# Kernel tuning notes

Hardware: AMD Instinct MI355X
Metric: run time of the kernel (lower is better)

## Reference

```python
import jax, jax.numpy as jnp
import numpy as np

FEATURE_DIM = 128  # user_aae.feature_dim == item_aae.feature_dim


def _encode(row, W1, b1, W2, b2):
    # row = [feature | x_rest]; original concatenates x and feature before the encoder MLP
    feat = row[:, :FEATURE_DIM]
    xr = row[:, FEATURE_DIM:]
    h = jax.nn.relu(jnp.concatenate([xr, feat], axis=-1) @ W1 + b1)
    return h @ W2 + b2  # [B, latent]


def setup_inputs() -> dict:
    key = jax.random.key(0)
    ks = jax.random.split(key, 12)
    B, NU, NI = 8192, 50000, 50000
    ROW, H, L = 2128, 512, 256  # feature_dim(128) + x_dim(2000)
    x = jnp.stack([
        jax.random.randint(ks[0], (B,), 0, NU),
        jax.random.randint(ks[1], (B,), 0, NI),
    ], axis=1).astype(jnp.int64)
    s1 = 1.0 / np.sqrt(ROW)
    s2 = 1.0 / np.sqrt(H)
    return {
        "x": x,
        "user_lookup": jax.random.normal(ks[2], (NU, ROW), jnp.float32),
        "item_lookup": jax.random.normal(ks[3], (NI, ROW), jnp.float32),
        "uW1": jax.random.normal(ks[4], (ROW, H), jnp.float32) * s1,
        "ub1": jnp.zeros((H,), jnp.float32),
        "uW2": jax.random.normal(ks[5], (H, L), jnp.float32) * s2,
        "ub2": jnp.zeros((L,), jnp.float32),
        "iW1": jax.random.normal(ks[6], (ROW, H), jnp.float32) * s1,
        "ib1": jnp.zeros((H,), jnp.float32),
        "iW2": jax.random.normal(ks[7], (H, L), jnp.float32) * s2,
        "ib2": jnp.zeros((L,), jnp.float32),
    }


def reference(x, user_lookup, item_lookup, uW1, ub1, uW2, ub2, iW1, ib1, iW2, ib2):
    user_row = user_lookup[x[:, 0]]  # [B, ROW]
    item_row = item_lookup[x[:, 1]]  # [B, ROW]
    u = _encode(user_row, uW1, ub1, uW2, ub2)  # [B, L]
    v = _encode(item_row, iW1, ib1, iW2, ib2)  # [B, L]
    # diag(u @ v.T) == rowwise dot product (identical math, no B x B matrix)
    diag = jnp.sum(u * v, axis=-1)
    return diag[:, None]  # [B, 1]
```

## Files before the change

kernel.cpp:

```cpp
#include <hip/hip_runtime.h>
#include <stdint.h>

typedef __attribute__((ext_vector_type(8))) short bf16x8;
typedef __attribute__((ext_vector_type(4))) float f32x4;

#define MFMA16(a, b, c) __builtin_amdgcn_mfma_f32_16x16x32_bf16((a), (b), (c), 0, 0, 0)

static __device__ __forceinline__ unsigned short f2bf(float f) {
  union { float f; unsigned int u; } cv;
  cv.f = f;
  return (unsigned short)((cv.u + 0x7fffu + ((cv.u >> 16) & 1u)) >> 16);
}

#define BATCH 8192
#define ROWD  2128
#define HID   512
#define LATD  256
#define KC1   272
#define NT1   68
#define HSL_TW (BATCH * HID)

__global__ __launch_bounds__(256) void ASAECF_tcast(
    const float* __restrict__ in0, const float* __restrict__ in1,
    unsigned short* __restrict__ out, int N, int lgN, int Kin, int KC, int perm)
{
  const float* __restrict__ in = blockIdx.z ? in1 : in0;
  unsigned short* __restrict__ o = out + (size_t)blockIdx.z * KC * N * 8;
  const int s = blockIdx.x * 256 + threadIdx.x;
  const int kc = s >> lgN, n = s & (N - 1);
  unsigned short v[8];
#pragma unroll
  for (int e = 0; e < 8; ++e) {
    const int k = kc * 8 + e;
    float f = 0.0f;
    if (k < Kin) {
      const int src = perm ? (k < 128 ? k + 2000 : k - 128) : k;
      f = in[(size_t)src * N + n];
    }
    v[e] = f2bf(f);
  }
  *(uint4*)(o + (size_t)s * 8) = *(const uint4*)v;
}

__global__ __launch_bounds__(512) void ASAECF_gemm1(
    const int* __restrict__ x,
    const float* __restrict__ ulook, const float* __restrict__ ilook,
    const unsigned short* __restrict__ w1s,
    const float* __restrict__ ub1, const float* __restrict__ ib1,
    unsigned short* __restrict__ hsl)
{
  const int bid   = blockIdx.x;
  const int xcd   = bid & 7;
  const int tower = xcd >> 2;
  const int rb    = (bid >> 3) * 4 + (xcd & 3);

  const float* __restrict__ look = tower ? ilook : ulook;
  const unsigned short* __restrict__ w1 = w1s + (size_t)tower * KC1 * HID * 8;
  const float* __restrict__ b1 = tower ? ib1 : ub1;
  unsigned short* __restrict__ hout = hsl + (size_t)tower * HSL_TW;

  __shared__ unsigned short Ab[2][64 * 40];

  const int tid  = threadIdx.x;
  const int lane = tid & 63, wid = tid >> 6;
  const int fr   = lane & 15, fq = lane >> 4;
  const int row0 = rb * 64;

  const int ar = tid >> 3, ak = (tid & 7) * 4;
  const long long arow = (long long)x[(row0 + ar) * 2 + tower] * ROWD + ak;

  int boff[4];
#pragma unroll
  for (int n = 0; n < 4; ++n)
    boff[n] = (fq * 512 + wid * 64 + n * 16 + fr) * 8;

  auto loadA = [&](int tt) -> f32x4 {
    f32x4 v = {0.0f, 0.0f, 0.0f, 0.0f};
    if (tt * 32 + ak <= ROWD - 4)
      v = __builtin_nontemporal_load((const f32x4*)(look + arow + tt * 32));
    return v;
  };
  auto writeA = [&](int buf, f32x4 v) {
    uint2 p;
    p.x = (unsigned)f2bf(v[0]) | ((unsigned)f2bf(v[1]) << 16);
    p.y = (unsigned)f2bf(v[2]) | ((unsigned)f2bf(v[3]) << 16);
    *(uint2*)&Ab[buf][ar * 40 + ak] = p;
  };

  f32x4 acc[4][4] = {};
  bf16x8 bgc[4], bgn[4];
  f32x4 rA0, rA1;

  writeA(0, loadA(0));
  rA0 = loadA(1);
  rA1 = loadA(2);
#pragma unroll
  for (int n = 0; n < 4; ++n) bgc[n] = *(const bf16x8*)(w1 + boff[n]);

#pragma unroll 2
  for (int t = 0; t < NT1; ++t) {
    __syncthreads();
    const int cu = t & 1;

    const unsigned short* bpn = w1 + (size_t)(t + 1) * (4 * 512 * 8);
#pragma unroll
    for (int n = 0; n < 4; ++n) bgn[n] = *(const bf16x8*)(bpn + boff[n]);

    bf16x8 af[4];
#pragma unroll
    for (int m = 0; m < 4; ++m)
      af[m] = *(const bf16x8*)&Ab[cu][(m * 16 + fr) * 40 + fq * 8];
#pragma unroll
    for (int n = 0; n < 4; ++n)
#pragma unroll
      for (int m = 0; m < 4; ++m)
        acc[m][n] = MFMA16(af[m], bgc[n], acc[m][n]);

    if (cu == 0) { writeA(1, rA0); rA0 = loadA(t + 3); }
    else         { writeA(0, rA1); rA1 = loadA(t + 3); }

#pragma unroll
    for (int n = 0; n < 4; ++n) bgc[n] = bgn[n];
  }

#pragma unroll
  for (int n = 0; n < 4; ++n) {
    const int col = wid * 64 + n * 16 + fr;
    const int kc = col >> 3, e = col & 7;
    const float bb = b1[col];
    unsigned short* hb = hout + (((size_t)rb * 64 + kc) * 64) * 8 + e;
#pragma unroll
    for (int m = 0; m < 4; ++m)
#pragma unroll
      for (int i = 0; i < 4; ++i) {
        const int row = m * 16 + fq * 4 + i;
        const float v = fmaxf(acc[m][n][i] + bb, 0.0f);
        hb[row * 8] = f2bf(v);
      }
  }
}

__global__ __launch_bounds__(512, 2) void ASAECF_gemm2dot(
    const unsigned short* __restrict__ hsl,
    const unsigned short* __restrict__ w2s,
    const float* __restrict__ ub2, const float* __restrict__ ib2,
    float* __restrict__ out)
{
  const int tid  = threadIdx.x;
  const int lane = tid & 63, wid = tid >> 6;
  const int fr   = lane & 15, fq = lane >> 4;
  const int rb   = blockIdx.x;
  const int row0 = rb * 32;

  const unsigned short* __restrict__ hu = hsl;
  const unsigned short* __restrict__ hv = hsl + (size_t)HSL_TW;
  const size_t abase = ((size_t)(rb >> 1) * 64) * 64 * 8;
  const int lrow0 = (rb & 1) * 32;

  f32x4 au[2][2] = {}, av[2][2] = {};

#pragma unroll
  for (int t = 0; t < 8; ++t) {
#pragma unroll
    for (int s = 0; s < 2; ++s) {
      const int kc = t * 8 + s * 4 + fq;
      bf16x8 a_u[2], a_v[2], b_u[2], b_v[2];
#pragma unroll
      for (int m = 0; m < 2; ++m) {
        const size_t off = abase + ((size_t)kc * 64 + lrow0 + m * 16 + fr) * 8;
        a_u[m] = *(const bf16x8*)(hu + off);
        a_v[m] = *(const bf16x8*)(hv + off);
      }
#pragma unroll
      for (int n = 0; n < 2; ++n) {
        const int col = wid * 32 + n * 16 + fr;
        const size_t offb = ((size_t)kc * 256 + col) * 8;
        b_u[n] = *(const bf16x8*)(w2s + offb);
        b_v[n] = *(const bf16x8*)(w2s + (size_t)64 * 256 * 8 + offb);
      }
#pragma unroll
      for (int m = 0; m < 2; ++m)
#pragma unroll
        for (int n = 0; n < 2; ++n) {
          au[m][n] = MFMA16(a_u[m], b_u[n], au[m][n]);
          av[m][n] = MFMA16(a_v[m], b_v[n], av[m][n]);
        }
    }
  }

  __shared__ float red[8][32];
  float bu[2], bv[2];
#pragma unroll
  for (int n = 0; n < 2; ++n) {
    const int col = wid * 32 + n * 16 + fr;
    bu[n] = ub2[col];
    bv[n] = ib2[col];
  }
#pragma unroll
  for (int m = 0; m < 2; ++m)
#pragma unroll
    for (int i = 0; i < 4; ++i) {
      float p = 0.0f;
#pragma unroll
      for (int n = 0; n < 2; ++n)
        p += (au[m][n][i] + bu[n]) * (av[m][n][i] + bv[n]);
      p += __shfl_xor(p, 1, 64);
      p += __shfl_xor(p, 2, 64);
      p += __shfl_xor(p, 4, 64);
      p += __shfl_xor(p, 8, 64);
      if (fr == 0) red[wid][m * 16 + fq * 4 + i] = p;
    }
  __syncthreads();
  if (tid < 32) {
    float s = 0.0f;
#pragma unroll
    for (int w = 0; w < 8; ++w) s += red[w][tid];
    out[row0 + tid] = s;
  }
}

extern "C" void kernel_launch(void* const* d_in, const int* in_sizes, int n_in,
                              void* d_out, int out_size, void* d_ws, size_t ws_size,
                              hipStream_t stream) {
  (void)in_sizes; (void)n_in; (void)out_size; (void)ws_size;
  const int*   x     = (const int*)d_in[0];
  const float* ulook = (const float*)d_in[1];
  const float* ilook = (const float*)d_in[2];
  const float* uW1   = (const float*)d_in[3];
  const float* ub1   = (const float*)d_in[4];
  const float* uW2   = (const float*)d_in[5];
  const float* ub2   = (const float*)d_in[6];
  const float* iW1   = (const float*)d_in[7];
  const float* ib1   = (const float*)d_in[8];
  const float* iW2   = (const float*)d_in[9];
  const float* ib2   = (const float*)d_in[10];
  float* out = (float*)d_out;

  char* ws = (char*)d_ws;
  unsigned short* w1s = (unsigned short*)(ws);
  unsigned short* w2s = (unsigned short*)(ws + 4456448);
  unsigned short* hsl = (unsigned short*)(ws + 4980736);

  ASAECF_tcast<<<dim3(544, 1, 2), 256, 0, stream>>>(uW1, iW1, w1s, 512, 9, ROWD, KC1, 1);
  ASAECF_tcast<<<dim3(64, 1, 2),  256, 0, stream>>>(uW2, iW2, w2s, 256, 8, HID, 64, 0);
  ASAECF_gemm1<<<dim3(256), 512, 0, stream>>>(x, ulook, ilook, w1s, ub1, ib1, hsl);
  ASAECF_gemm2dot<<<dim3(256), 512, 0, stream>>>(hsl, w2s, ub2, ib2, out);
}
```

Measured before the change: 89.37 us.

## Stage half-K gathered activation rows in large swizzled LDS before MFMA loop

The first GEMM now gathers all 64 rows of each block for half of the K range at once. It converts them to bf16 and stores them in about 136 KB of dynamic, XOR-swizzled LDS, then runs the MFMA loop over that half with no per-step barrier. This replaces the small double-buffered A tile, which needed a __syncthreads on every K step. The aim is more gather loads in flight and less barrier overhead. The cost is that the load and compute phases no longer overlap, and the large LDS footprint allows only one block per CU.

```diff
diff --git a/kernel.cpp b/kernel.cpp
--- a/kernel.cpp
+++ b/kernel.cpp
@@ -17,7 +17,9 @@
 #define HID   512
 #define LATD  256
 #define KC1   272
-#define NT1   68
+#define KHALF 1088
+#define KCH   136
+#define NTH   34
 #define HSL_TW (BATCH * HID)
 
 __global__ __launch_bounds__(256) void ASAECF_tcast(
@@ -49,6 +51,8 @@
     const float* __restrict__ ub1, const float* __restrict__ ib1,
     unsigned short* __restrict__ hsl)
 {
+  extern __shared__ unsigned short Asl[];
+
   const int bid   = blockIdx.x;
   const int xcd   = bid & 7;
   const int tower = xcd >> 2;
@@ -59,68 +63,80 @@
   const float* __restrict__ b1 = tower ? ib1 : ub1;
   unsigned short* __restrict__ hout = hsl + (size_t)tower * HSL_TW;
 
-  __shared__ unsigned short Ab[2][64 * 40];
-
   const int tid  = threadIdx.x;
   const int lane = tid & 63, wid = tid >> 6;
   const int fr   = lane & 15, fq = lane >> 4;
   const int row0 = rb * 64;
 
-  const int ar = tid >> 3, ak = (tid & 7) * 4;
-  const long long arow = (long long)x[(row0 + ar) * 2 + tower] * ROWD + ak;
+  const int rl = lane >> 4, kl = lane & 15;
+  const int r0 = wid * 4 + rl;
+  long long rbase[2];
+#pragma unroll
+  for (int p = 0; p < 2; ++p)
+    rbase[p] = (long long)x[(row0 + r0 + 32 * p) * 2 + tower] * ROWD;
 
   int boff[4];
 #pragma unroll
   for (int n = 0; n < 4; ++n)
     boff[n] = (fq * 512 + wid * 64 + n * 16 + fr) * 8;
 
-  auto loadA = [&](int tt) -> f32x4 {
-    f32x4 v = {0.0f, 0.0f, 0.0f, 0.0f};
-    if (tt * 32 + ak <= ROWD - 4)
-      v = __builtin_nontemporal_load((const f32x4*)(look + arow + tt * 32));
-    return v;
-  };
-  auto writeA = [&](int buf, f32x4 v) {
-    uint2 p;
-    p.x = (unsigned)f2bf(v[0]) | ((unsigned)f2bf(v[1]) << 16);
-    p.y = (unsigned)f2bf(v[2]) | ((unsigned)f2bf(v[3]) << 16);
-    *(uint2*)&Ab[buf][ar * 40 + ak] = p;
-  };
-
   f32x4 acc[4][4] = {};
-  bf16x8 bgc[4], bgn[4];
-  f32x4 rA0, rA1;
-
-  writeA(0, loadA(0));
-  rA0 = loadA(1);
-  rA1 = loadA(2);
-#pragma unroll
-  for (int n = 0; n < 4; ++n) bgc[n] = *(const bf16x8*)(w1 + boff[n]);
-
-#pragma unroll 2
-  for (int t = 0; t < NT1; ++t) {
+
+#pragma unroll
+  for (int h = 0; h < 2; ++h) {
+    if (h) __syncthreads();
+
+#pragma unroll
+    for (int p = 0; p < 2; ++p) {
+      const int r = r0 + 32 * p;
+      const float* rp = look + rbase[p] + h * KHALF;
+#pragma unroll
+      for (int s = 0; s < 9; ++s) {
+        const int klocal = kl * 8 + s * 128;
+        if (klocal < KHALF) {
+          const int gk = h * KHALF + klocal;
+          f32x4 a = {0.0f, 0.0f, 0.0f, 0.0f}, b = {0.0f, 0.0f, 0.0f, 0.0f};
+          if (gk + 8 <= ROWD) {
+            a = *(const f32x4*)(rp + klocal);
+            b = *(const f32x4*)(rp + klocal + 4);
+          }
+          unsigned short v[8];
+          v[0] = f2bf(a[0]); v[1] = f2bf(a[1]); v[2] = f2bf(a[2]); v[3] = f2bf(a[3]);
+          v[4] = f2bf(b[0]); v[5] = f2bf(b[1]); v[6] = f2bf(b[2]); v[7] = f2bf(b[3]);
+          const int kc = klocal >> 3;
+          const int slot = kc * 64 + (r ^ (kc & 7));
+          *(bf16x8*)&Asl[slot * 8] = *(const bf16x8*)v;
+        }
+      }
+    }
     __syncthreads();
-    const int cu = t & 1;
-
-    const unsigned short* bpn = w1 + (size_t)(t + 1) * (4 * 512 * 8);
-#pragma unroll
-    for (int n = 0; n < 4; ++n) bgn[n] = *(const bf16x8*)(bpn + boff[n]);
-
-    bf16x8 af[4];
-#pragma unroll
-    for (int m = 0; m < 4; ++m)
-      af[m] = *(const bf16x8*)&Ab[cu][(m * 16 + fr) * 40 + fq * 8];
-#pragma unroll
-    for (int n = 0; n < 4; ++n)
-#pragma unroll
-      for (int m = 0; m < 4; ++m)
-        acc[m][n] = MFMA16(af[m], bgc[n], acc[m][n]);
-
-    if (cu == 0) { writeA(1, rA0); rA0 = loadA(t + 3); }
-    else         { writeA(0, rA1); rA1 = loadA(t + 3); }
-
-#pragma unroll
-    for (int n = 0; n < 4; ++n) bgc[n] = bgn[n];
+
+    bf16x8 bgc[4], bgn[4];
+    const unsigned short* bp0 = w1 + (size_t)(h * NTH) * (4 * 512 * 8);
+#pragma unroll
+    for (int n = 0; n < 4; ++n) bgc[n] = *(const bf16x8*)(bp0 + boff[n]);
+
+    for (int tt = 0; tt < NTH; ++tt) {
+      const unsigned short* bpn = w1 + (size_t)(h * NTH + tt + 1) * (4 * 512 * 8);
+#pragma unroll
+      for (int n = 0; n < 4; ++n) bgn[n] = *(const bf16x8*)(bpn + boff[n]);
+
+      bf16x8 af[4];
+#pragma unroll
+      for (int m = 0; m < 4; ++m) {
+        const int kc = tt * 4 + fq;
+        const int slot = kc * 64 + ((m * 16 + fr) ^ (kc & 7));
+        af[m] = *(const bf16x8*)&Asl[slot * 8];
+      }
+#pragma unroll
+      for (int n = 0; n < 4; ++n)
+#pragma unroll
+        for (int m = 0; m < 4; ++m)
+          acc[m][n] = MFMA16(af[m], bgc[n], acc[m][n]);
+
+#pragma unroll
+      for (int n = 0; n < 4; ++n) bgc[n] = bgn[n];
+    }
   }
 
 #pragma unroll
@@ -243,6 +259,6 @@
 
   ASAECF_tcast<<<dim3(544, 1, 2), 256, 0, stream>>>(uW1, iW1, w1s, 512, 9, ROWD, KC1, 1);
   ASAECF_tcast<<<dim3(64, 1, 2),  256, 0, stream>>>(uW2, iW2, w2s, 256, 8, HID, 64, 0);
-  ASAECF_gemm1<<<dim3(256), 512, 0, stream>>>(x, ulook, ilook, w1s, ub1, ib1, hsl);
+  ASAECF_gemm1<<<dim3(256), 512, 139264, stream>>>(x, ulook, ilook, w1s, ub1, ib1, hsl);
   ASAECF_gemm2dot<<<dim3(256), 512, 0, stream>>>(hsl, w2s, ub2, ib2, out);
 }
```

Result: slower. 92.95 us (+4.0%).

## Retile gemm1 to 128-row by 256-col blocks with 2x4 warp grid

Applied to the files above, without the earlier changes.

Changes gemm1 block tiling from 64 rows by 512 columns to 128 rows by 256 columns, with waves laid out 2x4 over M and N. Each block now gathers 128 lookup rows (8 floats per thread) but only half of W1's columns. The gathered fp32 lookup data is then read by two blocks instead of one, trading more A reads for halved B traffic per block and better balance. It also drops the nontemporal hint on the A loads, so the second block reading the same rows can hit in L2, and it remaps blocks to XCDs so that pairs sharing rows stay on the same die.

```diff
diff --git a/kernel.cpp b/kernel.cpp
--- a/kernel.cpp
+++ b/kernel.cpp
@@ -51,45 +51,57 @@
 {
   const int bid   = blockIdx.x;
   const int xcd   = bid & 7;
+  const int idx   = bid >> 3;
   const int tower = xcd >> 2;
-  const int rb    = (bid >> 3) * 4 + (xcd & 3);
+  const int nh    = idx & 1;
+  const int mb    = (xcd & 3) * 16 + (idx >> 1);
 
   const float* __restrict__ look = tower ? ilook : ulook;
   const unsigned short* __restrict__ w1 = w1s + (size_t)tower * KC1 * HID * 8;
   const float* __restrict__ b1 = tower ? ib1 : ub1;
   unsigned short* __restrict__ hout = hsl + (size_t)tower * HSL_TW;
 
-  __shared__ unsigned short Ab[2][64 * 40];
+  __shared__ unsigned short Ab[2][128 * 40];
 
   const int tid  = threadIdx.x;
   const int lane = tid & 63, wid = tid >> 6;
+  const int wm   = wid >> 2, wn = wid & 3;
   const int fr   = lane & 15, fq = lane >> 4;
-  const int row0 = rb * 64;
-
-  const int ar = tid >> 3, ak = (tid & 7) * 4;
-  const long long arow = (long long)x[(row0 + ar) * 2 + tower] * ROWD + ak;
+  const int row0 = mb * 128;
+
+  const int ar  = tid >> 2;
+  const int ak8 = (tid & 3) * 8;
+  const long long arow = (long long)x[(row0 + ar) * 2 + tower] * ROWD + ak8;
 
   int boff[4];
 #pragma unroll
   for (int n = 0; n < 4; ++n)
-    boff[n] = (fq * 512 + wid * 64 + n * 16 + fr) * 8;
-
-  auto loadA = [&](int tt) -> f32x4 {
-    f32x4 v = {0.0f, 0.0f, 0.0f, 0.0f};
-    if (tt * 32 + ak <= ROWD - 4)
-      v = __builtin_nontemporal_load((const f32x4*)(look + arow + tt * 32));
+    boff[n] = (fq * 512 + nh * 256 + wn * 64 + n * 16 + fr) * 8;
+
+  struct A8 { f32x4 a, b; };
+  auto loadA = [&](int tt) -> A8 {
+    A8 v;
+    v.a = f32x4{0.0f, 0.0f, 0.0f, 0.0f};
+    v.b = f32x4{0.0f, 0.0f, 0.0f, 0.0f};
+    if (tt * 32 + ak8 + 8 <= ROWD) {
+      v.a = *(const f32x4*)(look + arow + tt * 32);
+      v.b = *(const f32x4*)(look + arow + tt * 32 + 4);
+    }
     return v;
   };
-  auto writeA = [&](int buf, f32x4 v) {
-    uint2 p;
-    p.x = (unsigned)f2bf(v[0]) | ((unsigned)f2bf(v[1]) << 16);
-    p.y = (unsigned)f2bf(v[2]) | ((unsigned)f2bf(v[3]) << 16);
-    *(uint2*)&Ab[buf][ar * 40 + ak] = p;
+  auto writeA = [&](int buf, A8 v) {
+    uint2 p, q;
+    p.x = (unsigned)f2bf(v.a[0]) | ((unsigned)f2bf(v.a[1]) << 16);
+    p.y = (unsigned)f2bf(v.a[2]) | ((unsigned)f2bf(v.a[3]) << 16);
+    q.x = (unsigned)f2bf(v.b[0]) | ((unsigned)f2bf(v.b[1]) << 16);
+    q.y = (unsigned)f2bf(v.b[2]) | ((unsigned)f2bf(v.b[3]) << 16);
+    *(uint2*)&Ab[buf][ar * 40 + ak8] = p;
+    *(uint2*)&Ab[buf][ar * 40 + ak8 + 4] = q;
   };
 
   f32x4 acc[4][4] = {};
   bf16x8 bgc[4], bgn[4];
-  f32x4 rA0, rA1;
+  A8 rA0, rA1;
 
   writeA(0, loadA(0));
   rA0 = loadA(1);
@@ -109,7 +121,7 @@
     bf16x8 af[4];
 #pragma unroll
     for (int m = 0; m < 4; ++m)
-      af[m] = *(const bf16x8*)&Ab[cu][(m * 16 + fr) * 40 + fq * 8];
+      af[m] = *(const bf16x8*)&Ab[cu][(wm * 64 + m * 16 + fr) * 40 + fq * 8];
 #pragma unroll
     for (int n = 0; n < 4; ++n)
 #pragma unroll
@@ -125,10 +137,11 @@
 
 #pragma unroll
   for (int n = 0; n < 4; ++n) {
-    const int col = wid * 64 + n * 16 + fr;
+    const int col = nh * 256 + wn * 64 + n * 16 + fr;
     const int kc = col >> 3, e = col & 7;
     const float bb = b1[col];
-    unsigned short* hb = hout + (((size_t)rb * 64 + kc) * 64) * 8 + e;
+    const int chunk = mb * 2 + wm;
+    unsigned short* hb = hout + (((size_t)chunk * 64 + kc) * 64) * 8 + e;
 #pragma unroll
     for (int m = 0; m < 4; ++m)
 #pragma unroll
```

Result: faster. 80.66 us (-9.8%).

## Warp-specialize gemm1 with a producer wave staging large swizzled A chunks

Applied to the files above, without the earlier changes.

gemm1 gets a dedicated ninth wave that gathers and converts 544-column chunks of the looked-up rows into a double-buffered, XOR-swizzled LDS tile (about 136 KB dynamic shared memory). The eight compute waves run 17 MFMA steps per chunk with one barrier per chunk instead of one per 32-wide K step. The aim is to cut barrier overhead and overlap the gather with compute. The risks are that a single wave issuing all the global loads becomes the bandwidth bottleneck, and that the large LDS footprint limits the kernel to one block per CU. The block-to-row mapping across XCDs also changes.

```diff
diff --git a/kernel.cpp b/kernel.cpp
--- a/kernel.cpp
+++ b/kernel.cpp
@@ -6,10 +6,10 @@
 
 #define MFMA16(a, b, c) __builtin_amdgcn_mfma_f32_16x16x32_bf16((a), (b), (c), 0, 0, 0)
 
-static __device__ __forceinline__ unsigned short f2bf(float f) {
-  union { float f; unsigned int u; } cv;
+static __device__ __forceinline__ unsigned f2bf(float f) {
+  union { float f; unsigned u; } cv;
   cv.f = f;
-  return (unsigned short)((cv.u + 0x7fffu + ((cv.u >> 16) & 1u)) >> 16);
+  return (cv.u + 0x7fffu + ((cv.u >> 16) & 1u)) >> 16;
 }
 
 #define BATCH 8192
@@ -17,7 +17,10 @@
 #define HID   512
 #define LATD  256
 #define KC1   272
-#define NT1   68
+#define KQ    544
+#define KCQ   68
+#define NTQ   17
+#define ABUF  (KCQ * 64 * 8)
 #define HSL_TW (BATCH * HID)
 
 __global__ __launch_bounds__(256) void ASAECF_tcast(
@@ -37,106 +40,116 @@
       const int src = perm ? (k < 128 ? k + 2000 : k - 128) : k;
       f = in[(size_t)src * N + n];
     }
-    v[e] = f2bf(f);
+    v[e] = (unsigned short)f2bf(f);
   }
   *(uint4*)(o + (size_t)s * 8) = *(const uint4*)v;
 }
 
-__global__ __launch_bounds__(512) void ASAECF_gemm1(
+__global__ __launch_bounds__(576) void ASAECF_gemm1(
     const int* __restrict__ x,
     const float* __restrict__ ulook, const float* __restrict__ ilook,
     const unsigned short* __restrict__ w1s,
     const float* __restrict__ ub1, const float* __restrict__ ib1,
     unsigned short* __restrict__ hsl)
 {
+  extern __shared__ unsigned short Asl[];
+
   const int bid   = blockIdx.x;
   const int xcd   = bid & 7;
   const int tower = xcd >> 2;
-  const int rb    = (bid >> 3) * 4 + (xcd & 3);
+  const int mb    = (xcd & 3) * 32 + (bid >> 3);
 
   const float* __restrict__ look = tower ? ilook : ulook;
   const unsigned short* __restrict__ w1 = w1s + (size_t)tower * KC1 * HID * 8;
   const float* __restrict__ b1 = tower ? ib1 : ub1;
   unsigned short* __restrict__ hout = hsl + (size_t)tower * HSL_TW;
 
-  __shared__ unsigned short Ab[2][64 * 40];
-
   const int tid  = threadIdx.x;
   const int lane = tid & 63, wid = tid >> 6;
   const int fr   = lane & 15, fq = lane >> 4;
-  const int row0 = rb * 64;
-
-  const int ar = tid >> 3, ak = (tid & 7) * 4;
-  const long long arow = (long long)x[(row0 + ar) * 2 + tower] * ROWD + ak;
+  const int row0 = mb * 64;
+
+  auto stage = [&](int q, int buf) {
+    unsigned short* Aq = Asl + buf * ABUF;
+#pragma unroll 4
+    for (int r = 0; r < 64; ++r) {
+      const long long ab = (long long)x[(row0 + r) * 2 + tower] * ROWD;
+      const float* rp = look + ab + q * KQ;
+#pragma unroll
+      for (int c = 0; c < 3; ++c) {
+        const int kl = c * 256 + lane * 4;
+        if (c < 2 || lane < 8) {
+          f32x4 v = {0.0f, 0.0f, 0.0f, 0.0f};
+          if (q * KQ + kl + 4 <= ROWD) v = *(const f32x4*)(rp + kl);
+          uint2 p;
+          p.x = f2bf(v[0]) | (f2bf(v[1]) << 16);
+          p.y = f2bf(v[2]) | (f2bf(v[3]) << 16);
+          const int kc = kl >> 3;
+          *(uint2*)&Aq[(kc * 64 + (r ^ (kc & 7))) * 8 + (lane & 1) * 4] = p;
+        }
+      }
+    }
+  };
 
   int boff[4];
 #pragma unroll
   for (int n = 0; n < 4; ++n)
     boff[n] = (fq * 512 + wid * 64 + n * 16 + fr) * 8;
-
-  auto loadA = [&](int tt) -> f32x4 {
-    f32x4 v = {0.0f, 0.0f, 0.0f, 0.0f};
-    if (tt * 32 + ak <= ROWD - 4)
-      v = __builtin_nontemporal_load((const f32x4*)(look + arow + tt * 32));
-    return v;
-  };
-  auto writeA = [&](int buf, f32x4 v) {
-    uint2 p;
-    p.x = (unsigned)f2bf(v[0]) | ((unsigned)f2bf(v[1]) << 16);
-    p.y = (unsigned)f2bf(v[2]) | ((unsigned)f2bf(v[3]) << 16);
-    *(uint2*)&Ab[buf][ar * 40 + ak] = p;
-  };
-
   f32x4 acc[4][4] = {};
-  bf16x8 bgc[4], bgn[4];
-  f32x4 rA0, rA1;
-
-  writeA(0, loadA(0));
-  rA0 = loadA(1);
-  rA1 = loadA(2);
-#pragma unroll
-  for (int n = 0; n < 4; ++n) bgc[n] = *(const bf16x8*)(w1 + boff[n]);
-
-#pragma unroll 2
-  for (int t = 0; t < NT1; ++t) {
+
+  if (wid == 8) stage(0, 0);
+  __syncthreads();
+
+  for (int q = 0; q < 4; ++q) {
+    if (wid == 8) {
+      if (q < 3) stage(q + 1, (q + 1) & 1);
+    } else {
+      const unsigned short* bq = w1 + (size_t)(q * NTQ) * (4 * 512 * 8);
+      const unsigned short* Aq = Asl + (q & 1) * ABUF;
+      bf16x8 bgc[4], bgn[4];
+#pragma unroll
+      for (int n = 0; n < 4; ++n) bgc[n] = *(const bf16x8*)(bq + boff[n]);
+      for (int tt = 0; tt < NTQ; ++tt) {
+        const int tn = (q * NTQ + tt + 1 <= 67) ? tt + 1 : tt;
+        const unsigned short* bpn = bq + (size_t)tn * (4 * 512 * 8);
+#pragma unroll
+        for (int n = 0; n < 4; ++n) bgn[n] = *(const bf16x8*)(bpn + boff[n]);
+
+        bf16x8 af[4];
+#pragma unroll
+        for (int m = 0; m < 4; ++m) {
+          const int kc = tt * 4 + fq;
+          af[m] = *(const bf16x8*)&Aq[(kc * 64 + ((m * 16 + fr) ^ (kc & 7))) * 8];
+        }
+#pragma unroll
+        for (int n = 0; n < 4; ++n)
+#pragma unroll
+          for (int m = 0; m < 4; ++m)
+            acc[m][n] = MFMA16(af[m], bgc[n], acc[m][n]);
+
+#pragma unroll
+        for (int n = 0; n < 4; ++n) bgc[n] = bgn[n];
+      }
+    }
     __syncthreads();
-    const int cu = t & 1;
-
-    const unsigned short* bpn = w1 + (size_t)(t + 1) * (4 * 512 * 8);
-#pragma unroll
-    for (int n = 0; n < 4; ++n) bgn[n] = *(const bf16x8*)(bpn + boff[n]);
-
-    bf16x8 af[4];
-#pragma unroll
-    for (int m = 0; m < 4; ++m)
-      af[m] = *(const bf16x8*)&Ab[cu][(m * 16 + fr) * 40 + fq * 8];
-#pragma unroll
-    for (int n = 0; n < 4; ++n)
+  }
+
+  if (wid < 8) {
+#pragma unroll
+    for (int n = 0; n < 4; ++n) {
+      const int col = wid * 64 + n * 16 + fr;
+      const int kc = col >> 3, e = col & 7;
+      const float bb = b1[col];
+      unsigned short* hb = hout + (((size_t)mb * 64 + kc) * 64) * 8 + e;
 #pragma unroll
       for (int m = 0; m < 4; ++m)
-        acc[m][n] = MFMA16(af[m], bgc[n], acc[m][n]);
-
-    if (cu == 0) { writeA(1, rA0); rA0 = loadA(t + 3); }
-    else         { writeA(0, rA1); rA1 = loadA(t + 3); }
-
-#pragma unroll
-    for (int n = 0; n < 4; ++n) bgc[n] = bgn[n];
-  }
-
-#pragma unroll
-  for (int n = 0; n < 4; ++n) {
-    const int col = wid * 64 + n * 16 + fr;
-    const int kc = col >> 3, e = col & 7;
-    const float bb = b1[col];
-    unsigned short* hb = hout + (((size_t)rb * 64 + kc) * 64) * 8 + e;
-#pragma unroll
-    for (int m = 0; m < 4; ++m)
-#pragma unroll
-      for (int i = 0; i < 4; ++i) {
-        const int row = m * 16 + fq * 4 + i;
-        const float v = fmaxf(acc[m][n][i] + bb, 0.0f);
-        hb[row * 8] = f2bf(v);
-      }
+#pragma unroll
+        for (int i = 0; i < 4; ++i) {
+          const int row = m * 16 + fq * 4 + i;
+          const float v = fmaxf(acc[m][n][i] + bb, 0.0f);
+          hb[row * 8] = (unsigned short)f2bf(v);
+        }
+    }
   }
 }
 
@@ -243,6 +256,6 @@
 
   ASAECF_tcast<<<dim3(544, 1, 2), 256, 0, stream>>>(uW1, iW1, w1s, 512, 9, ROWD, KC1, 1);
   ASAECF_tcast<<<dim3(64, 1, 2),  256, 0, stream>>>(uW2, iW2, w2s, 256, 8, HID, 64, 0);
-  ASAECF_gemm1<<<dim3(256), 512, 0, stream>>>(x, ulook, ilook, w1s, ub1, ib1, hsl);
+  ASAECF_gemm1<<<dim3(256), 576, 139264, stream>>>(x, ulook, ilook, w1s, ub1, ib1, hsl);
   ASAECF_gemm2dot<<<dim3(256), 512, 0, stream>>>(hsl, w2s, ub2, ib2, out);
 }
```

After: 274.9 us. +207.6%, slower.
